# Performance work log

Hardware: AMD Instinct MI355X
Metric: run time of the kernel (lower is better)

The kernel has to match this reference:

```python
import jax, jax.numpy as jnp
import numpy as np

B, N, DIM = 4, 1024, 512
DEPTH, HEADS, DH = 4, 8, 64
INNER = HEADS * DH  # 512
W = 32              # sqrt(N), FeedForward reshapes tokens to (W, W)
SCALE = DH ** -0.5  # used for BOTH spatial and spectral branches (as in source)
EPS_LN = 1e-5
EPS_BN = 1e-5


def setup_inputs() -> dict:
    key = jax.random.key(0)
    ks = jax.random.split(key, 16)
    L = DEPTH
    def rn(k, shape, s=0.02):
        return jax.random.normal(k, shape, jnp.float32) * s
    return {
        "x": jax.random.normal(ks[0], (B, N, DIM), jnp.float32),
        "ln1_w": jnp.ones((L, DIM), jnp.float32), "ln1_b": jnp.zeros((L, DIM), jnp.float32),
        "Wqkv": rn(ks[1], (L, DIM, 3 * INNER)),
        "Wout": rn(ks[2], (L, INNER, DIM)), "bout": jnp.zeros((L, DIM), jnp.float32),
        "sp_w": rn(ks[3], (L, HEADS, HEADS, 3, 3), 0.1), "sp_b": jnp.zeros((L, HEADS), jnp.float32),
        "Wqkv_spec": rn(ks[4], (L, N, 3 * N)),
        "spec_w": rn(ks[5], (L, 1, 1, 3, 3), 0.1), "spec_b": jnp.zeros((L, 1), jnp.float32),
        "ln2_w": jnp.ones((L, DIM), jnp.float32), "ln2_b": jnp.zeros((L, DIM), jnp.float32),
        "dw_w": rn(ks[6], (L, DIM, 1, 3, 3), 0.1), "dw_b": jnp.zeros((L, DIM), jnp.float32),
        "pw_w": rn(ks[7], (L, 256, DIM)), "pw_b": jnp.zeros((L, 256), jnp.float32),
        "bn_g": jnp.ones((L, 256), jnp.float32), "bn_b": jnp.zeros((L, 256), jnp.float32),
        "bn_m": jnp.zeros((L, 256), jnp.float32), "bn_v": jnp.ones((L, 256), jnp.float32),
        "c1_w": rn(ks[8], (L, 512, 256)), "c1_b": jnp.zeros((L, 512), jnp.float32),
        "c2_w": rn(ks[9], (L, DIM, 512)), "c2_b": jnp.zeros((L, DIM), jnp.float32),
    }


def _ln(x, w, b):
    mu = x.mean(-1, keepdims=True)
    var = x.var(-1, keepdims=True)  # biased, matching torch LayerNorm
    return (x - mu) * jax.lax.rsqrt(var + EPS_LN) * w + b


def _conv3x3(x, w, b, groups=1):
    y = jax.lax.conv_general_dilated(x, w, (1, 1), 'SAME',
                                     dimension_numbers=('NCHW', 'OIHW', 'NCHW'),
                                     feature_group_count=groups)
    return y + b[None, :, None, None]


def _block(x, p):
    (ln1w, ln1b, Wqkv, Wout, bout, spw, spb, Wqs, scw, scb,
     ln2w, ln2b, dww, dwb, pww, pwb, bng, bnb, bnm, bnv, c1w, c1b, c2w, c2b) = p
    b = x.shape[0]
    # --- spatial attention (PreNorm) ---
    h = _ln(x, ln1w, ln1b)
    q, k, v = jnp.split(h @ Wqkv, 3, axis=-1)
    split_heads = lambda t: t.reshape(b, N, HEADS, DH).transpose(0, 2, 1, 3)  # b h n d
    q, k, v = split_heads(q), split_heads(k), split_heads(v)
    attn = jax.nn.softmax(jnp.einsum('bhid,bhjd->bhij', q, k) * SCALE, axis=-1)
    attn = _conv3x3(attn, spw, spb)  # conv over the softmax map (heads as channels)
    out = jnp.einsum('bhij,bhjd->bhid', attn, v).transpose(0, 2, 1, 3).reshape(b, N, INNER)
    out = out @ Wout + bout  # (b, n, dim)
    # --- spectral attention on h^T (b, dim, n); v_spec is dead code in source ---
    xt = jnp.swapaxes(h, -1, -2)
    qs, ks_, _vs = jnp.split(xt @ Wqs, 3, axis=-1)  # each (b, dim, n)
    a = jax.nn.softmax(jnp.einsum('bin,bjn->bij', qs, ks_) * SCALE, axis=-1)
    a = _conv3x3(a[:, None], scw, scb)[:, 0]  # (b, dim, dim)
    x = x + jnp.einsum('bnd,bde->bne', out, a)  # residual add from Transformer loop
    # --- FeedForward (PreNorm), FF adds its own internal residual too ---
    h2 = _ln(x, ln2w, ln2b)
    img = h2.reshape(b, W, W, DIM).transpose(0, 3, 1, 2)  # 'b (w h) c -> b c w h'
    t = _conv3x3(img, dww, dwb, groups=DIM)               # depthwise 3x3
    t = jnp.einsum('oc,bchw->bohw', pww, t) + pwb[None, :, None, None]  # pointwise dim->256
    t = (t - bnm[None, :, None, None]) * jax.lax.rsqrt(bnv + EPS_BN)[None, :, None, None] \
        * bng[None, :, None, None] + bnb[None, :, None, None]           # BatchNorm2d (eval)
    t = jax.nn.gelu(jnp.einsum('oc,bchw->bohw', c1w, t) + c1b[None, :, None, None], approximate=False)
    t = jax.nn.gelu(jnp.einsum('oc,bchw->bohw', c2w, t) + c2b[None, :, None, None], approximate=False)
    ff = h2 + t.transpose(0, 2, 3, 1).reshape(b, N, DIM)  # FF internal residual
    return x + ff


def _forward(x, ln1_w, ln1_b, Wqkv, Wout, bout, sp_w, sp_b, Wqkv_spec, spec_w, spec_b,
             ln2_w, ln2_b, dw_w, dw_b, pw_w, pw_b, bn_g, bn_b, bn_m, bn_v,
             c1_w, c1_b, c2_w, c2_b):
    stacked = (ln1_w, ln1_b, Wqkv, Wout, bout, sp_w, sp_b, Wqkv_spec, spec_w, spec_b,
               ln2_w, ln2_b, dw_w, dw_b, pw_w, pw_b, bn_g, bn_b, bn_m, bn_v,
               c1_w, c1_b, c2_w, c2_b)
    for i in range(DEPTH):
        x = _block(x, tuple(a[i] for a in stacked))
    return x


def reference(x, ln1_w, ln1_b, Wqkv, Wout, bout, sp_w, sp_b, Wqkv_spec, spec_w, spec_b,
              ln2_w, ln2_b, dw_w, dw_b, pw_w, pw_b, bn_g, bn_b, bn_m, bn_v,
              c1_w, c1_b, c2_w, c2_b):
    return _forward(x, ln1_w, ln1_b, Wqkv, Wout, bout, sp_w, sp_b, Wqkv_spec, spec_w, spec_b,
                    ln2_w, ln2_b, dw_w, dw_b, pw_w, pw_b, bn_g, bn_b, bn_m, bn_v,
                    c1_w, c1_b, c2_w, c2_b)
```

## Files before the change

### kernel.cpp

```cpp
#include <hip/hip_runtime.h>
#include <hip/hip_bf16.h>

typedef __hip_bfloat16 bf16;
typedef __attribute__((ext_vector_type(8))) short bf16x8;
typedef __attribute__((ext_vector_type(4))) float f32x4;

__device__ __forceinline__ float b2f(bf16 v){ return __bfloat162float(v); }
__device__ __forceinline__ bf16 f2b(float v){ return __float2bfloat16(v); }
__device__ __forceinline__ float bits2f(unsigned u){ return __uint_as_float(u << 16); }
__device__ __forceinline__ unsigned short f2bits(float v){ bf16 t = __float2bfloat16(v); return *(unsigned short*)&t; }

__device__ __forceinline__ float gelu_f(float x){
  return 0.5f * x * (1.f + erff(x * 0.7071067811865475f));
}

__device__ __forceinline__ void gload_lds(const void* g, void* l){
  __builtin_amdgcn_global_load_lds((const __attribute__((address_space(1))) void*)g,
                                   (__attribute__((address_space(3))) void*)l, 16, 0, 0);
}

template<bool MAX>
__device__ __forceinline__ float block_reduce(float v){
  __shared__ float s[4];
  #pragma unroll
  for (int o = 32; o > 0; o >>= 1){
    float t = __shfl_down(v, o, 64);
    v = MAX ? fmaxf(v, t) : (v + t);
  }
  int lane = threadIdx.x & 63, w = threadIdx.x >> 6;
  __syncthreads();
  if (lane == 0) s[w] = v;
  __syncthreads();
  return MAX ? fmaxf(fmaxf(s[0], s[1]), fmaxf(s[2], s[3]))
             : (s[0] + s[1] + s[2] + s[3]);
}

__global__ void detect_k(const unsigned* __restrict__ x, int* __restrict__ flag){
  __shared__ int cnt[256];
  int tid = threadIdx.x;
  int c = 0;
  for (int i = tid; i < 4096; i += 256){
    unsigned h = x[i] & 0xffffu;
    int e = (int)((h >> 7) & 0xff);
    if (h == 0u || (e >= 100 && e <= 133)) c++;
  }
  cnt[tid] = c;
  __syncthreads();
  for (int o = 128; o > 0; o >>= 1){ if (tid < o) cnt[tid] += cnt[tid+o]; __syncthreads(); }
  if (tid == 0) *flag = (cnt[0] < 2048) ? 1 : 0;
}

__global__ __launch_bounds__(256) void cvt_x_k(const void* __restrict__ src,
                                               float* __restrict__ X,
                                               const int* __restrict__ flag){
  int p = blockIdx.x*256 + threadIdx.x;
  X[p] = (*flag) ? ((const float*)src)[p]
                 : __bfloat162float(((const bf16*)src)[p]);
}

struct WCvt21 { const void* src[21]; long long cum[22]; };

__global__ __launch_bounds__(256) void cvt_w_k(WCvt21 a, bf16* __restrict__ WB,
                                               long long total, const int* __restrict__ flag){
  long long i = (long long)blockIdx.x*256 + threadIdx.x;
  if (i >= total) return;
  int t = 0;
  while (a.cum[t+1] <= i) t++;
  long long e = i - a.cum[t];
  WB[i] = (*flag) ? __float2bfloat16(((const float*)a.src[t])[e])
                  : ((const bf16*)a.src[t])[e];
}

__global__ __launch_bounds__(256) void wtrans_k(const void* __restrict__ src, bf16* __restrict__ dst,
                                                int ld_src, int ldd, long long sSrc, long long sDst,
                                                const int* __restrict__ flag){
  __shared__ bf16 t[64][65];
  int z = blockIdx.z;
  int r0 = blockIdx.x*64, c0 = blockIdx.y*64;
  int lane = threadIdx.x & 63, quad = threadIdx.x >> 6;
  const float* sf = (const float*)src;
  const bf16* sb = (const bf16*)src;
  int fl = *flag;
  #pragma unroll
  for (int k = 0; k < 16; ++k){
    int r = quad*16 + k;
    long long idx = z*sSrc + (long long)(r0+r)*ld_src + c0 + lane;
    float v = fl ? sf[idx] : b2f(sb[idx]);
    t[r][lane] = f2b(v);
  }
  __syncthreads();
  #pragma unroll
  for (int k = 0; k < 16; ++k){
    int c = quad*16 + k;
    dst[z*sDst + (long long)(c0+c)*ldd + r0 + lane] = t[lane][c];
  }
}

__global__ void wprep_k(const bf16* __restrict__ spw, bf16* __restrict__ Wr){
  int l = blockIdx.x;
  for (int t = threadIdx.x; t < 1536; t += 256){
    int ho = t / 96, k = t - ho*96;
    float v = 0.f;
    if (ho < 8 && k < 72){
      int tap = k >> 3, hi = k & 7;
      v = b2f(spw[l*576 + ho*72 + hi*9 + tap]);
    }
    Wr[l*1536 + t] = f2b(v);
  }
}

__global__ __launch_bounds__(256) void store_out_k(const float* __restrict__ X,
                                                   void* __restrict__ out,
                                                   const int* __restrict__ flag){
  int p = blockIdx.x*256 + threadIdx.x;
  if (*flag) ((float*)out)[p] = X[p];
  else       ((bf16*)out)[p] = f2b(X[p]);
}

__global__ __launch_bounds__(256) void zero_k(float* __restrict__ p, int n){
  int i = blockIdx.x*256 + threadIdx.x;
  if (i < n) p[i] = 0.f;
}

template<int MF, int NF, typename TC, int EXP>
__global__ __launch_bounds__(256) void gmfma_k(
    int M, int N, int K,
    const bf16* __restrict__ A, int lda, long long sA, long long sA2,
    const bf16* __restrict__ Bt, int ldb, long long sB, long long sB2,
    TC* __restrict__ C, int ldc, long long sC, long long sC2,
    float alpha, int beta,
    const bf16* __restrict__ bias_n,
    const float* __restrict__ scale_n,
    const float* __restrict__ shift_n,
    const bf16* __restrict__ addF,
    int act,
    bf16* __restrict__ vt,
    float* __restrict__ srow, long long szl, long long szh, long long sgm)
{
  constexpr int BM = MF*32, BN = NF*32;
  constexpr int CHA = BM/16, CH = (BM+BN)/16;
  static_assert(CH % 4 == 0, "chunks must divide among 4 waves");
  __shared__ bf16 Asm[BM][32];
  __shared__ bf16 Bsm[BN][32];
  const int tid = threadIdx.x;
  const int lane = tid & 63, wid = tid >> 6;
  const int wm = wid >> 1, wn = wid & 1;
  const int m0 = blockIdx.y*BM, n0 = blockIdx.x*BN;
  const int z = blockIdx.z;
  const long long zl = z & 7, zh = z >> 3;
  const bf16* Ab = A + zl*sA + zh*sA2;
  const bf16* Bb = Bt + zl*sB + zh*sB2;
  TC* Cb = C + zl*sC + zh*sC2;
  const bf16* Fb = addF ? addF + zl*sC + zh*sC2 : nullptr;

  f32x4 acc[MF][NF];
  f32x4 zero = {0.f, 0.f, 0.f, 0.f};
  #pragma unroll
  for (int m = 0; m < MF; ++m)
    #pragma unroll
    for (int n = 0; n < NF; ++n) acc[m][n] = zero;

  const int rchunk = lane >> 2;
  const int kchunk = (lane & 3) * 8;
  const int row16 = lane & 15, kq = (lane >> 4) * 8;

  for (int k0 = 0; k0 < K; k0 += 32){
    #pragma unroll
    for (int cc = 0; cc < CH/4; ++cc){
      int c = wid + cc*4;
      if (c < CHA){
        int row = c*16 + rchunk;
        gload_lds(Ab + (long long)(m0+row)*lda + k0 + kchunk, &Asm[c*16][0]);
      } else {
        int row = (c-CHA)*16 + rchunk;
        gload_lds(Bb + (long long)(n0+row)*ldb + k0 + kchunk, &Bsm[(c-CHA)*16][0]);
      }
    }
    __syncthreads();
    bf16x8 af[MF], bfr[NF];
    #pragma unroll
    for (int m = 0; m < MF; ++m)
      af[m] = *(const bf16x8*)&Asm[wm*(MF*16) + m*16 + row16][kq];
    #pragma unroll
    for (int n = 0; n < NF; ++n)
      bfr[n] = *(const bf16x8*)&Bsm[wn*(NF*16) + n*16 + row16][kq];
    #pragma unroll
    for (int m = 0; m < MF; ++m)
      #pragma unroll
      for (int n = 0; n < NF; ++n)
        acc[m][n] = __builtin_amdgcn_mfma_f32_16x16x32_bf16(af[m], bfr[n], acc[m][n], 0, 0, 0);
    __syncthreads();
  }

  if constexpr (EXP){
    #pragma unroll
    for (int m = 0; m < MF; ++m){
      int gmb = m0 + wm*(MF*16) + m*16 + (lane >> 4)*4;
      float rowsum[4] = {0.f, 0.f, 0.f, 0.f};
      #pragma unroll
      for (int n = 0; n < NF; ++n){
        int gn = n0 + wn*(NF*16) + n*16 + row16;
        #pragma unroll
        for (int r = 0; r < 4; ++r){
          float e = __expf(acc[m][n][r] * alpha);
          long long idx = (long long)(gmb + r)*ldc + gn;
          if constexpr (__is_same(TC, float)) Cb[idx] = e; else Cb[idx] = f2b(e);
          rowsum[r] += e;
        }
      }
      #pragma unroll
      for (int r = 0; r < 4; ++r){
        float s = rowsum[r];
        #pragma unroll
        for (int o = 1; o < 16; o <<= 1) s += __shfl_xor(s, o, 64);
        if ((lane & 15) == 0)
          atomicAdd(&srow[zl*szl + zh*szh + (long long)(gmb + r)*sgm], s);
      }
    }
    return;
  }

  #pragma unroll
  for (int m = 0; m < MF; ++m){
    #pragma unroll
    for (int n = 0; n < NF; ++n){
      int gn = n0 + wn*(NF*16) + n*16 + row16;
      float bn_ = bias_n ? b2f(bias_n[gn]) : 0.f;
      float sc = scale_n ? scale_n[gn] : 1.f;
      float sh = shift_n ? shift_n[gn] : 0.f;
      int gmb = m0 + wm*(MF*16) + m*16 + (lane >> 4)*4;
      float vals[4];
      #pragma unroll
      for (int r = 0; r < 4; ++r){
        int gm = gmb + r;
        float v = acc[m][n][r] * alpha + bn_;
        v = v * sc + sh;
        if (act) v = gelu_f(v);
        long long idx = (long long)gm*ldc + gn;
        if (Fb) v += b2f(Fb[idx]);
        if (beta){
          float old;
          if constexpr (__is_same(TC, float)) old = Cb[idx]; else old = b2f(Cb[idx]);
          v += old;
        }
        if constexpr (__is_same(TC, float)) Cb[idx] = v; else Cb[idx] = f2b(v);
        vals[r] = v;
      }
      if (vt && gn >= 1024){
        int h = (gn - 1024) >> 6, d = (gn - 1024) & 63;
        int bb = gmb >> 10, nn = gmb & 1023;
        ushort4 o;
        o.x = f2bits(vals[0]); o.y = f2bits(vals[1]);
        o.z = f2bits(vals[2]); o.w = f2bits(vals[3]);
        *(ushort4*)&vt[(((long long)bb*8 + h)*64 + d)*1024 + nn] = o;
      }
    }
  }
}

template<int MF, int NF, typename TC>
static void gmfma_x(hipStream_t st, int z, int M, int N, int K,
                    const bf16* A, int lda, long long sA, long long sA2,
                    const bf16* Bt, int ldb, long long sB, long long sB2,
                    TC* C, int ldc, long long sC, long long sC2,
                    float alpha = 1.f, int beta = 0,
                    const bf16* bias_n = nullptr,
                    const float* scale_n = nullptr, const float* shift_n = nullptr,
                    const bf16* addF = nullptr, int act = 0, bf16* vt = nullptr)
{
  dim3 g(N/(NF*32), M/(MF*32), z);
  gmfma_k<MF,NF,TC,0><<<g, 256, 0, st>>>(M,N,K,A,lda,sA,sA2,Bt,ldb,sB,sB2,C,ldc,sC,sC2,
                                         alpha,beta,bias_n,scale_n,shift_n,addF,act,vt,
                                         nullptr,0,0,0);
}

template<int MF, int NF, typename TC>
static void gmfma(hipStream_t st, int z, int M, int N, int K,
                  const bf16* A, int lda, long long sA,
                  const bf16* Bt, int ldb, long long sB,
                  TC* C, int ldc, long long sC,
                  float alpha = 1.f, int beta = 0,
                  const bf16* bias_n = nullptr,
                  const float* scale_n = nullptr, const float* shift_n = nullptr,
                  const bf16* addF = nullptr, int act = 0, bf16* vt = nullptr)
{
  gmfma_x<MF,NF,TC>(st, z, M, N, K, A, lda, sA, 8*sA, Bt, ldb, sB, 8*sB,
                    C, ldc, sC, 8*sC, alpha, beta, bias_n, scale_n, shift_n, addF, act, vt);
}

template<int MF, int NF, typename TC>
static void gmfma_exp(hipStream_t st, int z, int M, int N, int K,
                      const bf16* A, int lda, long long sA, long long sA2,
                      const bf16* Bt, int ldb, long long sB, long long sB2,
                      TC* C, int ldc, long long sC, long long sC2,
                      float alpha,
                      float* srow, long long szl, long long szh, long long sgm)
{
  dim3 g(N/(NF*32), M/(MF*32), z);
  gmfma_k<MF,NF,TC,1><<<g, 256, 0, st>>>(M,N,K,A,lda,sA,sA2,Bt,ldb,sB,sB2,C,ldc,sC,sC2,
                                         alpha,0,nullptr,nullptr,nullptr,nullptr,0,nullptr,
                                         srow,szl,szh,sgm);
}

__global__ __launch_bounds__(256) void ln_k(const float* __restrict__ X, bf16* __restrict__ Y,
                                            const bf16* __restrict__ w, const bf16* __restrict__ b){
  long long row = blockIdx.x;
  const float* x = X + row*512;
  bf16* y = Y + row*512;
  int tid = threadIdx.x;
  float v0 = x[tid], v1 = x[tid+256];
  float mean = block_reduce<false>(v0+v1) * (1.f/512.f);
  float msq  = block_reduce<false>(v0*v0+v1*v1) * (1.f/512.f);
  float var = msq - mean*mean;
  float rs = rsqrtf(var + 1e-5f);
  y[tid]     = f2b((v0-mean)*rs*b2f(w[tid])     + b2f(b[tid]));
  y[tid+256] = f2b((v1-mean)*rs*b2f(w[tid+256]) + b2f(b[tid+256]));
}

__device__ __forceinline__ int csw(int col){ return col ^ ((col >> 3) & 7); }

__global__ __launch_bounds__(256) void convNorm_k(
    const bf16* __restrict__ Sp, bf16* __restrict__ Pout,
    const bf16* __restrict__ Wr, const bf16* __restrict__ bias,
    const float* __restrict__ Srow,
    long long bstride)
{
  __shared__ bf16 tile[10][66][8];
  __shared__ float irow[10][8];
  long long b = blockIdx.z;
  int i0 = blockIdx.y*8;
  int jh0 = blockIdx.x*512;
  int tid = threadIdx.x;
  const bf16* src = Sp + b*bstride;

  if (tid < 80){
    int r = tid >> 3, h = tid & 7;
    int gi = i0 + r - 1;
    float iv = 0.f;
    if ((unsigned)gi < 1024u) iv = 1.f / Srow[(b*1024 + gi)*8 + h];
    irow[r][h] = iv;
  }

  int lane = tid & 63, wid = tid >> 6;
  int row16 = lane & 15, q = lane >> 4;
  bf16x8 wf0 = *(const bf16x8*)&Wr[row16*96 +  0 + q*8];
  bf16x8 wf1 = *(const bf16x8*)&Wr[row16*96 + 32 + q*8];
  bf16x8 wf2 = *(const bf16x8*)&Wr[row16*96 + 64 + q*8];
  float bv = (row16 < 8) ? b2f(bias[row16]) : 0.f;

  for (int c = 0; c < 8; ++c){
    int base = jh0 + c*64;
    __syncthreads();
    for (int t = tid; t < 320; t += 256){
      int row = t >> 5, rem = t & 31;
      int hp = rem >> 3, seg = rem & 7;
      int gi = i0 + row - 1;
      int g0 = base + seg*8;
      unsigned ov[8];
      if ((unsigned)gi < 1024u){
        const bf16* p0 = src + (long long)(2*hp)*1048576 + (long long)gi*1024 + g0;
        bf16x8 a0 = *(const bf16x8*)p0;
        bf16x8 a1 = *(const bf16x8*)(p0 + 1048576);
        float i0v = irow[row][2*hp];
        float i1v = irow[row][2*hp+1];
        #pragma unroll
        for (int k = 0; k < 8; ++k){
          float e0 = bits2f((unsigned)(unsigned short)a0[k]) * i0v;
          float e1 = bits2f((unsigned)(unsigned short)a1[k]) * i1v;
          ov[k] = (unsigned)f2bits(e0) | ((unsigned)f2bits(e1) << 16);
        }
      } else {
        #pragma unroll
        for (int k = 0; k < 8; ++k) ov[k] = 0u;
      }
      #pragma unroll
      for (int k = 0; k < 8; ++k)
        *(unsigned*)&tile[row][csw(1 + seg*8 + k)][2*hp] = ov[k];
    }
    if (tid < 40){
      int row = tid >> 2, hp = tid & 3;
      int gi = i0 + row - 1;
      unsigned L = 0u, R = 0u;
      if ((unsigned)gi < 1024u){
        long long rb = (long long)gi*1024;
        int cl = base - 1, cr = base + 64;
        float i0v = irow[row][2*hp];
        float i1v = irow[row][2*hp+1];
        if (cl >= 0){
          float e0 = b2f(src[(long long)(2*hp)*1048576 + rb + cl]) * i0v;
          float e1 = b2f(src[(long long)(2*hp+1)*1048576 + rb + cl]) * i1v;
          L = (unsigned)f2bits(e0) | ((unsigned)f2bits(e1) << 16);
        }
        if (cr < 1024){
          float e0 = b2f(src[(long long)(2*hp)*1048576 + rb + cr]) * i0v;
          float e1 = b2f(src[(long long)(2*hp+1)*1048576 + rb + cr]) * i1v;
          R = (unsigned)f2bits(e0) | ((unsigned)f2bits(e1) << 16);
        }
      }
      *(unsigned*)&tile[row][csw(0)][2*hp] = L;
      *(unsigned*)&tile[row][csw(65)][2*hp] = R;
    }
    __syncthreads();
    #pragma unroll
    for (int rr = 0; rr < 2; ++rr){
      int ii = rr*4 + wid;
      f32x4 zero = {0.f,0.f,0.f,0.f};
      f32x4 acc[4] = {zero,zero,zero,zero};
      #pragma unroll
      for (int ks = 0; ks < 3; ++ks){
        int tap = ks*4 + q;
        int tcl = tap > 8 ? 0 : tap;
        int di = tcl/3, dj = tcl - di*3;
        bf16x8 wsel = ks==0 ? wf0 : (ks==1 ? wf1 : wf2);
        #pragma unroll
        for (int mf = 0; mf < 4; ++mf){
          bf16x8 af = *(const bf16x8*)&tile[ii+di][csw(mf*16 + row16 + dj)][0];
          acc[mf] = __builtin_amdgcn_mfma_f32_16x16x32_bf16(af, wsel, acc[mf], 0, 0, 0);
        }
      }
      if (row16 < 8){
        bf16* dst = Pout + b*bstride + (long long)row16*1048576 + (long long)(i0+ii)*1024;
        #pragma unroll
        for (int mf = 0; mf < 4; ++mf){
          int j = base + mf*16 + q*4;
          ushort4 o;
          o.x = f2bits(acc[mf][0] + bv);
          o.y = f2bits(acc[mf][1] + bv);
          o.z = f2bits(acc[mf][2] + bv);
          o.w = f2bits(acc[mf][3] + bv);
          *(ushort4*)&dst[j] = o;
        }
      }
    }
  }
}

__global__ __launch_bounds__(256) void conv_spec_k(const float* __restrict__ in, bf16* __restrict__ out,
                                                   const bf16* __restrict__ w, const bf16* __restrict__ bias,
                                                   const float* __restrict__ SSrow){
  __shared__ float ti[66][67];
  __shared__ bf16 toutT[64][65];
  __shared__ float sis[66];
  int b = blockIdx.z;
  int i0 = blockIdx.y*64, j0 = blockIdx.x*64;
  int tid = threadIdx.x;
  const float* ib = in + (long long)b*262144;
  if (tid < 66){
    int gi = i0 + tid - 1;
    float iv = 0.f;
    if ((unsigned)gi < 512u) iv = 1.f / SSrow[b*512 + gi];
    sis[tid] = iv;
  }
  __syncthreads();
  for (int t = tid; t < 66*66; t += 256){
    int r = t / 66, cc = t - r*66;
    int gi = i0 + r - 1, gj = j0 + cc - 1;
    float v = 0.f;
    if ((unsigned)gi < 512u && (unsigned)gj < 512u)
      v = ib[gi*512 + gj] * sis[r];
    ti[r][cc] = v;
  }
  __syncthreads();
  float w9[9], bv = b2f(bias[0]);
  #pragma unroll
  for (int d = 0; d < 9; ++d) w9[d] = b2f(w[d]);
  int ii = tid & 63;
  #pragma unroll
  for (int q = 0; q < 16; ++q){
    int jj = (tid >> 6)*16 + q;
    float acc = bv;
    #pragma unroll
    for (int di = 0; di < 3; ++di)
      #pragma unroll
      for (int dj = 0; dj < 3; ++dj)
        acc += w9[di*3+dj] * ti[ii+di][jj+dj];
    toutT[jj][ii] = f2b(acc);
  }
  __syncthreads();
  #pragma unroll
  for (int q = 0; q < 16; ++q){
    int jj = (tid >> 6)*16 + q;
    out[(long long)b*262144 + (j0+jj)*512 + i0 + (tid & 63)] = toutT[jj][tid & 63];
  }
}

__global__ __launch_bounds__(256) void dwconv_k(const bf16* __restrict__ H2, bf16* __restrict__ T1,
                                                const bf16* __restrict__ w, const bf16* __restrict__ bias){
  int p = blockIdx.x*256 + threadIdx.x;
  int cp = p & 255;
  int n = (p >> 8) & 1023;
  int b = p >> 18;
  int c0 = cp*2;
  int wi = n >> 5, hg = n & 31;
  float a0 = b2f(bias[c0]), a1 = b2f(bias[c0+1]);
  #pragma unroll
  for (int di = 0; di < 3; ++di){
    int gw = wi + di - 1;
    if ((unsigned)gw >= 32u) continue;
    #pragma unroll
    for (int dj = 0; dj < 3; ++dj){
      int gh = hg + dj - 1;
      if ((unsigned)gh >= 32u) continue;
      unsigned hv = *(const unsigned*)&H2[((long long)b*1024 + (gw*32+gh))*512 + c0];
      float w0 = b2f(w[c0*9 + di*3 + dj]);
      float w1 = b2f(w[(c0+1)*9 + di*3 + dj]);
      a0 += w0 * bits2f(hv & 0xffffu);
      a1 += w1 * bits2f(hv >> 16);
    }
  }
  bf16 h0 = f2b(a0), h1 = f2b(a1);
  unsigned o = ((unsigned)*(unsigned short*)&h1 << 16) | (unsigned)*(unsigned short*)&h0;
  *(unsigned*)&T1[((long long)b*1024 + n)*512 + c0] = o;
}

__global__ void bnaff_all_k(const bf16* __restrict__ pwb, const bf16* __restrict__ g,
                            const bf16* __restrict__ bb, const bf16* __restrict__ m,
                            const bf16* __restrict__ v, float* __restrict__ BNAFF){
  int l = blockIdx.x, o = threadIdx.x;
  float s = b2f(g[l*256+o]) * rsqrtf(b2f(v[l*256+o]) + 1e-5f);
  BNAFF[l*512 + o] = s;
  BNAFF[l*512 + 256 + o] = (b2f(pwb[l*256+o]) - b2f(m[l*256+o])) * s + b2f(bb[l*256+o]);
}

__global__ __launch_bounds__(256) void htrans_k(const bf16* __restrict__ Hb, bf16* __restrict__ HT){
  __shared__ bf16 t[64][65];
  int b = blockIdx.z;
  int n0 = blockIdx.x*64, c0 = blockIdx.y*64;
  int lane = threadIdx.x & 63, quad = threadIdx.x >> 6;
  #pragma unroll
  for (int k = 0; k < 16; ++k){
    int r = quad*16 + k;
    t[r][lane] = Hb[((long long)b*1024 + n0 + r)*512 + c0 + lane];
  }
  __syncthreads();
  #pragma unroll
  for (int k = 0; k < 16; ++k){
    int c = quad*16 + k;
    HT[(long long)b*524288 + (long long)(c0+c)*1024 + n0 + lane] = t[lane][c];
  }
}

extern "C" void kernel_launch(void* const* d_in, const int* in_sizes, int n_in,
                              void* d_out, int out_size, void* d_ws, size_t ws_size,
                              hipStream_t stream)
{
  (void)in_sizes; (void)n_in; (void)out_size;

  const bool big = ws_size >= 207000000ull;
  const long long ATTN_SZ = big ? 33554432LL : 8388608LL;

  float* X     = (float*)d_ws;
  bf16*  WBsm  = (bf16*)(X + 2097152);
  bf16*  WqkvT = WBsm  + 2139648;
  bf16*  WoutT = WqkvT + 3145728;
  bf16*  WqsT  = WoutT + 1048576;
  bf16*  Hbuf  = WqsT  + 8388608;
  bf16*  HbufT = Hbuf  + 2097152;
  bf16*  QKV   = HbufT + 2097152;
  bf16*  Vt    = QKV   + 6291456;
  bf16*  OUTH  = Vt    + 2097152;
  bf16*  OUT   = OUTH  + 2097152;
  bf16*  ATTN  = OUT   + 2097152;
  bf16*  ATTNC = ATTN  + ATTN_SZ;
  float* BNAFF = (float*)(ATTNC + ATTN_SZ);
  bf16*  WR    = (bf16*)(BNAFF + 2048);
  float* SROW  = (float*)(WR + 6144);
  float* SSROW = SROW + 32768;
  int*   FLAG  = (int*)(SSROW + 2048);

  float* ASPEC   = (float*)OUTH;
  bf16*  ASPECCT = ATTNC;
  bf16*  T1 = ATTN;
  bf16*  T3 = ATTN + 2097152;
  bf16*  T2 = ATTNC + 2097152;
  bf16*  SQK = ATTN;

  static const int widx[21] = {1,2,5,6,7,9,10,11,12,13,14,15,16,17,18,19,20,21,22,23,24};
  static const long long wsz[21] = {2048,2048,2048,2304,32,36,4,2048,2048,18432,2048,
                                    524288,1024,1024,1024,1024,1024,524288,2048,1048576,2048};
  WCvt21 wc;
  long long cum = 0;
  bf16* wp[21];
  for (int t = 0; t < 21; ++t){
    wc.src[t] = d_in[widx[t]];
    wc.cum[t] = cum;
    wp[t] = WBsm + cum;
    cum += wsz[t];
  }
  wc.cum[21] = cum;

  bf16 *w_ln1w = wp[0],  *w_ln1b = wp[1],  *w_bout = wp[2],  *w_spw = wp[3];
  bf16 *w_spb  = wp[4],  *w_specw= wp[5],  *w_specb= wp[6],  *w_ln2w= wp[7];
  bf16 *w_ln2b = wp[8],  *w_dww  = wp[9],  *w_dwb  = wp[10], *w_pww = wp[11];
  bf16 *w_pwb  = wp[12], *w_bng  = wp[13], *w_bnb  = wp[14], *w_bnm = wp[15];
  bf16 *w_bnv  = wp[16], *w_c1w  = wp[17], *w_c1b  = wp[18], *w_c2w = wp[19];
  bf16 *w_c2b  = wp[20];

  detect_k<<<1, 256, 0, stream>>>((const unsigned*)d_in[0], FLAG);
  cvt_x_k<<<8192, 256, 0, stream>>>(d_in[0], X, FLAG);
  cvt_w_k<<<(int)((cum + 255)/256), 256, 0, stream>>>(wc, WBsm, cum, FLAG);
  wtrans_k<<<dim3(8,24,4), 256, 0, stream>>>(d_in[3], WqkvT, 1536, 512, 786432LL, 786432LL, FLAG);
  wtrans_k<<<dim3(8, 8,4), 256, 0, stream>>>(d_in[4], WoutT,  512, 512, 262144LL, 262144LL, FLAG);
  wtrans_k<<<dim3(16,32,4),256, 0, stream>>>(d_in[8], WqsT,  3072,1024, 3145728LL,2097152LL, FLAG);
  bnaff_all_k<<<4, 256, 0, stream>>>(w_pwb, w_bng, w_bnb, w_bnm, w_bnv, BNAFF);
  wprep_k<<<4, 256, 0, stream>>>(w_spw, WR);

  for (int l = 0; l < 4; ++l){
    zero_k<<<136, 256, 0, stream>>>(SROW, 34816);
    ln_k<<<4096, 256, 0, stream>>>(X, Hbuf, w_ln1w + l*512, w_ln1b + l*512);
    gmfma<4,4,bf16>(stream, 1, 4096, 1536, 512,
        Hbuf, 512, 0, WqkvT + (long long)l*786432, 512, 0, QKV, 1536, 0,
        1.f, 0, nullptr, nullptr, nullptr, nullptr, 0, Vt);
    if (big){
      gmfma_exp<4,4,bf16>(stream, 32, 1024, 1024, 64,
          QKV, 1536, 64, 1572864, QKV + 512, 1536, 64, 1572864,
          ATTN, 1024, 1048576, 8388608, 0.125f,
          SROW, 1, 8192, 8);
      convNorm_k<<<dim3(2,128,4), 256, 0, stream>>>(ATTN, ATTNC, WR + l*1536, w_spb + l*8,
                                                    SROW, 8388608LL);
      gmfma_x<2,2,bf16>(stream, 32, 1024, 64, 1024,
          ATTNC, 1024, 1048576, 8388608, Vt, 1024, 65536, 524288,
          OUTH, 512, 64, 524288);
    } else {
      for (int b = 0; b < 4; ++b){
        bf16* qkvb = QKV + (long long)b*1572864;
        gmfma_exp<4,4,bf16>(stream, 8, 1024, 1024, 64,
            qkvb, 1536, 64, 8*64, qkvb + 512, 1536, 64, 8*64,
            ATTN, 1024, 1048576, 8*1048576, 0.125f,
            SROW + b*8192, 1, 0, 8);
        convNorm_k<<<dim3(2,128,1), 256, 0, stream>>>(ATTN, ATTNC, WR + l*1536, w_spb + l*8,
                                                      SROW + b*8192, 8388608LL);
        gmfma<2,2,bf16>(stream, 8, 1024, 64, 1024,
            ATTNC, 1024, 1048576, Vt + (long long)b*524288, 1024, 65536,
            OUTH + (long long)b*524288, 512, 64);
      }
    }
    gmfma<2,2,bf16>(stream, 1, 4096, 512, 512,
        OUTH, 512, 0, WoutT + (long long)l*262144, 512, 0, OUT, 512, 0,
        1.f, 0, w_bout + l*512);
    htrans_k<<<dim3(16,8,4), 256, 0, stream>>>(Hbuf, HbufT);
    gmfma<4,4,bf16>(stream, 4, 512, 2048, 1024,
        HbufT, 1024, 524288, WqsT + (long long)l*2097152, 1024, 0, SQK, 2048, 1048576);
    gmfma_exp<2,2,float>(stream, 4, 512, 512, 1024,
        SQK, 2048, 1048576, 8*1048576, SQK + 1024, 2048, 1048576, 8*1048576,
        ASPEC, 512, 262144, 8*262144, 0.125f,
        SSROW, 512, 0, 1);
    conv_spec_k<<<dim3(8,8,4), 256, 0, stream>>>(ASPEC, ASPECCT, w_specw + l*9, w_specb + l,
                                                 SSROW);
    gmfma<2,2,float>(stream, 4, 1024, 512, 512,
        OUT, 512, 524288, ASPECCT, 512, 262144, X, 512, 524288, 1.f, 1);
    ln_k<<<4096, 256, 0, stream>>>(X, Hbuf, w_ln2w + l*512, w_ln2b + l*512);
    dwconv_k<<<4096, 256, 0, stream>>>(Hbuf, T1, w_dww + l*4608, w_dwb + l*512);
    gmfma<2,2,bf16>(stream, 4, 1024, 256, 512,
        T1, 512, 524288, w_pww + (long long)l*131072, 512, 0, T2, 256, 262144,
        1.f, 0, nullptr, BNAFF + l*512, BNAFF + l*512 + 256);
    gmfma<2,2,bf16>(stream, 4, 1024, 512, 256,
        T2, 256, 262144, w_c1w + (long long)l*131072, 256, 0, T3, 512, 524288,
        1.f, 0, w_c1b + l*512, nullptr, nullptr, nullptr, 1);
    gmfma<2,2,float>(stream, 4, 1024, 512, 512,
        T3, 512, 524288, w_c2w + (long long)l*262144, 512, 0, X, 512, 524288,
        1.f, 1, w_c2b + l*512, nullptr, nullptr, Hbuf, 1);
  }

  store_out_k<<<8192, 256, 0, stream>>>(X, d_out, FLAG);
}
```

Before: 1.202 ms.

## Fuse spatial attention conv-normalize with PV matmul into one kernel

Merges the 3x3 head-mixing conv over normalized attention scores with the subsequent attention-times-V matmul. Each block now processes a full 8-row strip across all 1024 columns, keeping the conv output in LDS and accumulating the P·V product in registers. This removes the write and re-read of the large ATTNC intermediate and one kernel launch. In exchange the grid halves to 512 blocks, LDS use grows, an extra barrier is added per chunk, and V is read directly from global memory without LDS staging.

```diff
diff --git a/kernel.cpp b/kernel.cpp
--- a/kernel.cpp
+++ b/kernel.cpp
@@ -319,17 +319,18 @@
 
 __device__ __forceinline__ int csw(int col){ return col ^ ((col >> 3) & 7); }
 
-__global__ __launch_bounds__(256) void convNorm_k(
-    const bf16* __restrict__ Sp, bf16* __restrict__ Pout,
+__global__ __launch_bounds__(256) void convPV_k(
+    const bf16* __restrict__ Sp,
     const bf16* __restrict__ Wr, const bf16* __restrict__ bias,
     const float* __restrict__ Srow,
+    const bf16* __restrict__ Vt, bf16* __restrict__ OUTH,
     long long bstride)
 {
   __shared__ bf16 tile[10][66][8];
   __shared__ float irow[10][8];
+  __shared__ unsigned short plds[8*1160];
   long long b = blockIdx.z;
   int i0 = blockIdx.y*8;
-  int jh0 = blockIdx.x*512;
   int tid = threadIdx.x;
   const bf16* src = Sp + b*bstride;
 
@@ -340,6 +341,10 @@
     if ((unsigned)gi < 1024u) iv = 1.f / Srow[(b*1024 + gi)*8 + h];
     irow[r][h] = iv;
   }
+  for (int t = tid; t < 8*8*72; t += 256){
+    int h = t / 576, rem = t - h*576;
+    plds[h*1160 + (8 + rem/72)*72 + (rem - (rem/72)*72)] = 0;
+  }
 
   int lane = tid & 63, wid = tid >> 6;
   int row16 = lane & 15, q = lane >> 4;
@@ -348,8 +353,16 @@
   bf16x8 wf2 = *(const bf16x8*)&Wr[row16*96 + 64 + q*8];
   float bv = (row16 < 8) ? b2f(bias[row16]) : 0.f;
 
-  for (int c = 0; c < 8; ++c){
-    int base = jh0 + c*64;
+  f32x4 zero4 = {0.f,0.f,0.f,0.f};
+  f32x4 pacc[2][4];
+  #pragma unroll
+  for (int hh = 0; hh < 2; ++hh)
+    #pragma unroll
+    for (int nf = 0; nf < 4; ++nf) pacc[hh][nf] = zero4;
+  int h0 = wid*2;
+
+  for (int c = 0; c < 16; ++c){
+    int base = c*64;
     __syncthreads();
     for (int t = tid; t < 320; t += 256){
       int row = t >> 5, rem = t & 31;
@@ -404,8 +417,7 @@
     #pragma unroll
     for (int rr = 0; rr < 2; ++rr){
       int ii = rr*4 + wid;
-      f32x4 zero = {0.f,0.f,0.f,0.f};
-      f32x4 acc[4] = {zero,zero,zero,zero};
+      f32x4 acc[4] = {zero4, zero4, zero4, zero4};
       #pragma unroll
       for (int ks = 0; ks < 3; ++ks){
         int tap = ks*4 + q;
@@ -419,19 +431,43 @@
         }
       }
       if (row16 < 8){
-        bf16* dst = Pout + b*bstride + (long long)row16*1048576 + (long long)(i0+ii)*1024;
+        unsigned short* pp = &plds[row16*1160 + ii*72];
         #pragma unroll
         for (int mf = 0; mf < 4; ++mf){
-          int j = base + mf*16 + q*4;
           ushort4 o;
           o.x = f2bits(acc[mf][0] + bv);
           o.y = f2bits(acc[mf][1] + bv);
           o.z = f2bits(acc[mf][2] + bv);
           o.w = f2bits(acc[mf][3] + bv);
-          *(ushort4*)&dst[j] = o;
-        }
-      }
-    }
+          *(ushort4*)&pp[mf*16 + q*4] = o;
+        }
+      }
+    }
+    __syncthreads();
+    #pragma unroll
+    for (int hh = 0; hh < 2; ++hh){
+      int h = h0 + hh;
+      const bf16* vb = Vt + (((long long)b*8 + h) << 16);
+      #pragma unroll
+      for (int ks = 0; ks < 2; ++ks){
+        bf16x8 af = *(const bf16x8*)&plds[h*1160 + row16*72 + ks*32 + q*8];
+        #pragma unroll
+        for (int nf = 0; nf < 4; ++nf){
+          bf16x8 bfv = *(const bf16x8*)&vb[(long long)(nf*16 + row16)*1024 + base + ks*32 + q*8];
+          pacc[hh][nf] = __builtin_amdgcn_mfma_f32_16x16x32_bf16(af, bfv, pacc[hh][nf], 0, 0, 0);
+        }
+      }
+    }
+  }
+  if (q < 2){
+    #pragma unroll
+    for (int hh = 0; hh < 2; ++hh)
+      #pragma unroll
+      for (int nf = 0; nf < 4; ++nf)
+        #pragma unroll
+        for (int r = 0; r < 4; ++r)
+          OUTH[((long long)b*1024 + i0 + q*4 + r)*512 + (h0+hh)*64 + nf*16 + row16] =
+              f2b(pacc[hh][nf][r]);
   }
 }
 
@@ -616,11 +652,8 @@
           QKV, 1536, 64, 1572864, QKV + 512, 1536, 64, 1572864,
           ATTN, 1024, 1048576, 8388608, 0.125f,
           SROW, 1, 8192, 8);
-      convNorm_k<<<dim3(2,128,4), 256, 0, stream>>>(ATTN, ATTNC, WR + l*1536, w_spb + l*8,
-                                                    SROW, 8388608LL);
-      gmfma_x<2,2,bf16>(stream, 32, 1024, 64, 1024,
-          ATTNC, 1024, 1048576, 8388608, Vt, 1024, 65536, 524288,
-          OUTH, 512, 64, 524288);
+      convPV_k<<<dim3(1,128,4), 256, 0, stream>>>(ATTN, WR + l*1536, w_spb + l*8,
+                                                  SROW, Vt, OUTH, 8388608LL);
     } else {
       for (int b = 0; b < 4; ++b){
         bf16* qkvb = QKV + (long long)b*1572864;
@@ -628,11 +661,9 @@
             qkvb, 1536, 64, 8*64, qkvb + 512, 1536, 64, 8*64,
             ATTN, 1024, 1048576, 8*1048576, 0.125f,
             SROW + b*8192, 1, 0, 8);
-        convNorm_k<<<dim3(2,128,1), 256, 0, stream>>>(ATTN, ATTNC, WR + l*1536, w_spb + l*8,
-                                                      SROW + b*8192, 8388608LL);
-        gmfma<2,2,bf16>(stream, 8, 1024, 64, 1024,
-            ATTNC, 1024, 1048576, Vt + (long long)b*524288, 1024, 65536,
-            OUTH + (long long)b*524288, 512, 64);
+        convPV_k<<<dim3(1,128,1), 256, 0, stream>>>(ATTN, WR + l*1536, w_spb + l*8,
+                                                    SROW + b*8192, Vt + (long long)b*524288,
+                                                    OUTH + (long long)b*524288, 8388608LL);
       }
     }
     gmfma<2,2,bf16>(stream, 1, 4096, 512, 512,
```

Result: slower. 1.385 ms (+15.2%).
